# Kernel tuning notes

Measured on AMD Instinct MI355X. Metric: run time of the kernel, lower is better.

Reference implementation:

```python
import jax, jax.numpy as jnp
import numpy as np

T, B = 128, 64
STATE_DIM, LATENT_DIM, AC_DIM, MS_DIM = 32, 16, 8, 8
STATE_EMBED, AC_EMBED, HIDDEN, OUT_DIM = 64, 16, 64, 18


def setup_inputs() -> dict:
    key = jax.random.key(0)
    ks = jax.random.split(key, 18)
    f = lambda i, shape: jax.random.normal(ks[i], shape, jnp.float32)
    s = 0.05  # param scale
    return dict(
        state=f(0, (T, B, STATE_DIM)),
        latent_mean=f(1, (T, B, LATENT_DIM)),
        latent_logvar=f(2, (T, B, LATENT_DIM)) * 0.1,
        latent_mean_t=f(3, (T, B, LATENT_DIM)),
        latent_logvar_t=f(4, (T, B, LATENT_DIM)) * 0.1,
        agent_character=f(5, (T, B, AC_DIM)),
        mental_state=f(6, (T, B, MS_DIM)),
        partner_actions=jax.random.randint(ks[7], (T, B), 0, OUT_DIM, jnp.int32),
        dones=(jax.random.uniform(ks[8], (T, B)) < 0.05).astype(jnp.float32),
        W_state=f(9, (STATE_DIM, STATE_EMBED)) * s, b_state=jnp.zeros(STATE_EMBED),
        W_ac=f(10, (AC_DIM, AC_EMBED)) * s, b_ac=jnp.zeros(AC_EMBED),
        W_embed=f(11, (STATE_EMBED + AC_EMBED, HIDDEN)) * s, b_embed=jnp.zeros(HIDDEN),
        W_hid=f(12, (AC_EMBED + MS_DIM, HIDDEN)) * s, b_hid=jnp.zeros(HIDDEN),
        Wi=f(13, (HIDDEN, 3 * HIDDEN)) * s, bi=jnp.zeros(3 * HIDDEN),
        Wh_rz=f(14, (HIDDEN, 2 * HIDDEN)) * s,
        Wh_n=f(15, (HIDDEN, HIDDEN)) * s, bh_n=jnp.zeros(HIDDEN),
        W_out=f(16, (HIDDEN, OUT_DIM)) * s, b_out=jnp.zeros(OUT_DIM),
    )


def reference(state, latent_mean, latent_logvar, latent_mean_t, latent_logvar_t,
              agent_character, mental_state, partner_actions, dones,
              W_state, b_state, W_ac, b_ac, W_embed, b_embed, W_hid, b_hid,
              Wi, bi, Wh_rz, Wh_n, bh_n, W_out, b_out):
    Tn = state.shape[0]
    # ---- KL between consecutive latent Gaussians (with N(0,I) prior at t=0) ----
    lm = jnp.concatenate((latent_mean, latent_mean_t), -1)      # (T,B,2L)
    lv = jnp.concatenate((latent_logvar, latent_logvar_t), -1)
    G = lm.shape[-1]
    am = jnp.concatenate((jnp.zeros((1,) + lm.shape[1:], lm.dtype), lm))
    al = jnp.concatenate((jnp.zeros((1,) + lv.shape[1:], lv.dtype), lv))
    mu, m = am[1:], am[:-1]
    logE, logS = al[1:], al[:-1]
    kl = 0.5 * (logS.sum(-1) - logE.sum(-1) - G
                + jnp.exp(logE - logS).sum(-1)
                + ((m - mu) ** 2 / jnp.exp(logS)).sum(-1))      # (T,B)
    kl_loss = kl.sum()
    # ---- feature extractors ----
    se = jax.nn.relu(state @ W_state + b_state)                 # (T,B,SE)
    ae = jax.nn.relu(agent_character @ W_ac + b_ac)             # (T,B,AE)
    embed = jnp.concatenate((se, ae), -1) @ W_embed + b_embed   # (T,B,H)
    hidden = jnp.concatenate((ae, mental_state), -1) @ W_hid + b_hid  # (T,B,H)
    # ---- k-batch: K=T shifted trajectories, zero-padded at the tail ----
    idx = jnp.arange(Tn)[:, None] + jnp.arange(Tn)[None, :]     # (K,T)
    valid = idx < Tn                                            # (K,T) bool
    cidx = jnp.minimum(idx, Tn - 1)
    vf = valid.astype(embed.dtype)[..., None]                   # (K,T,1)
    k_embed = embed[cidx] * vf[..., None]                       # (K,T,B,H)
    k_hidden = hidden[cidx] * vf[..., None]                     # (K,T,B,H)
    k_dones = dones[cidx] * vf                                  # (K,T,B)
    k_actions = jnp.where(valid[..., None], partner_actions[cidx], 0)  # (K,T,B)
    # fill_to_first_true: 1 up to and including the first done of each k-traj
    episode_mask = (jnp.cumsum(k_dones, axis=1) - k_dones == 0).astype(embed.dtype)  # (K,T,B)
    # ---- GRU scan over timestep axis, vectorized over (K,B) ----
    h0 = k_hidden[:, 0]                                         # (K,B,H)
    xs = (jnp.moveaxis(k_embed, 1, 0), jnp.moveaxis(k_hidden, 1, 0), jnp.moveaxis(k_dones, 1, 0))

    def step(h, x):
        x_t, h0_t, d_t = x                                      # (K,B,H),(K,B,H),(K,B)
        h = jnp.where(d_t[..., None] > 0, h0_t, h)              # reset on done
        ir, iz, i_n = jnp.split(x_t @ Wi + bi, 3, -1)
        hr, hz = jnp.split(h @ Wh_rz, 2, -1)
        r = jax.nn.sigmoid(ir + hr)
        z = jax.nn.sigmoid(iz + hz)
        n = jnp.tanh(i_n + r * (h @ Wh_n + bh_n))
        h_new = (1.0 - z) * n + z * h
        return h_new, h_new

    _, hs = jax.lax.scan(step, h0, xs)                          # (T,K,B,H)
    logp = jax.nn.log_softmax(hs @ W_out + b_out, -1)           # (T,K,B,O)
    k_act_t = jnp.moveaxis(k_actions, 1, 0)                     # (T,K,B)
    nll = -jnp.take_along_axis(logp, k_act_t[..., None], -1)[..., 0]  # (T,K,B)
    mask = valid.T[:, :, None].astype(nll.dtype) * jnp.moveaxis(episode_mask, 1, 0)
    recon_loss = (nll * mask).sum(axis=1)                       # sum over K -> (T,B)
    return kl_loss, recon_loss
```

## Files before the change

kernel.cpp:

```cpp
#include <hip/hip_runtime.h>


#define XI_OFF   0
#define HID_OFF  6291456
#define CTR_OFF  8388608

typedef float f32x16 __attribute__((ext_vector_type(16)));
typedef _Float16 h2 __attribute__((ext_vector_type(2)));

#if __has_builtin(__builtin_amdgcn_fdot2)
#define DOT2(a, b, c) __builtin_amdgcn_fdot2((a), (b), (c), false)
#else
#define DOT2(a, b, c) ((c) + (float)(a).x * (float)(b).x + (float)(a).y * (float)(b).y)
#endif

__device__ __forceinline__ h2 pack_pair(float h) {
  int hb = __builtin_bit_cast(int, h);
  int hp = __builtin_amdgcn_mov_dpp(hb, 0xB1, 0xF, 0xF, true);
  return __builtin_bit_cast(h2, __builtin_amdgcn_cvt_pkrtz(h, __builtin_bit_cast(float, hp)));
}

__global__ __launch_bounds__(256, 1) void precompute_kernel(
    const float* __restrict__ state, const float* __restrict__ ac, const float* __restrict__ ms,
    const float* __restrict__ Wst, const float* __restrict__ bst,
    const float* __restrict__ Wac, const float* __restrict__ bac,
    const float* __restrict__ Wem, const float* __restrict__ bem,
    const float* __restrict__ Whd, const float* __restrict__ bhd,
    const float* __restrict__ Wi,  const float* __restrict__ bi,
    const float* __restrict__ lm, const float* __restrict__ lv,
    const float* __restrict__ lmt, const float* __restrict__ lvt,
    float* __restrict__ xi, float* __restrict__ hid0, float* __restrict__ out) {
  __shared__ float sWst[32 * 64];
  __shared__ float sWem[80 * 64];
  __shared__ float sWhd[24 * 64];
  __shared__ float sWac[8 * 16];
  __shared__ float sb[208];
  __shared__ float sin_[4][48];
  __shared__ float sse[4][80];
  __shared__ float semb[4][64];
  __shared__ float ps[4];
  int tid = threadIdx.x, lane = tid & 63, w = tid >> 6;

  if (blockIdx.x >= 256) {
    float total = 0.f;
    for (int it = 0; it < 16; ++it) {
      int idx = ((int)blockIdx.x - 256) * 256 + tid + it * 16384;
      int g = idx & 31;
      int pair = idx >> 5;
      const float* M = (g < 16) ? lm : lmt;
      const float* V = (g < 16) ? lv : lvt;
      int cur = pair * 16 + (g & 15);
      float mu = M[cur], lE = V[cur];
      float m = 0.f, lS = 0.f;
      if (pair >= 64) { m = M[cur - 1024]; lS = V[cur - 1024]; }
      float d = m - mu;
      total += 0.5f * (lS - lE - 1.f + __expf(lE - lS) + d * d * __expf(-lS));
    }
    #pragma unroll
    for (int off = 32; off; off >>= 1) total += __shfl_xor(total, off);
    if (lane == 0) ps[w] = total;
    __syncthreads();
    if (tid == 0) atomicAdd(out, ps[0] + ps[1] + ps[2] + ps[3]);
    return;
  }

  f32x16 wi0[4], wi1[4], wi2[4];
  #pragma unroll
  for (int k = 0; k < 64; ++k) {
    wi0[k >> 4][k & 15] = Wi[k * 192 + lane];
    wi1[k >> 4][k & 15] = Wi[k * 192 + 64 + lane];
    wi2[k >> 4][k & 15] = Wi[k * 192 + 128 + lane];
  }
  for (int i = tid; i < 32 * 64; i += 256) sWst[i] = Wst[i];
  for (int i = tid; i < 80 * 64; i += 256) sWem[i] = Wem[i];
  for (int i = tid; i < 24 * 64; i += 256) sWhd[i] = Whd[i];
  for (int i = tid; i < 8 * 16; i += 256) sWac[i] = Wac[i];
  if (tid < 64) sb[tid] = bst[tid];
  if (tid < 16) sb[64 + tid] = bac[tid];
  if (tid < 64) sb[80 + tid] = bem[tid];
  if (tid < 64) sb[144 + tid] = bhd[tid];
  float bi0 = bi[lane], bi1 = bi[64 + lane], bi2 = bi[128 + lane];
  __syncthreads();
  for (int cnt = 0; cnt < 8; ++cnt) {
    int pair = blockIdx.x * 32 + w * 8 + cnt;
    if (lane < 32)      sin_[w][lane] = state[pair * 32 + lane];
    else if (lane < 40) sin_[w][lane] = ac[pair * 8 + (lane - 32)];
    else if (lane < 48) sin_[w][lane] = ms[pair * 8 + (lane - 40)];
    __syncthreads();
    float se = sb[lane];
    #pragma unroll
    for (int k = 0; k < 32; ++k) se += sin_[w][k] * sWst[k * 64 + lane];
    se = fmaxf(se, 0.f);
    float ae = 0.f;
    if (lane < 16) {
      ae = sb[64 + lane];
      #pragma unroll
      for (int k = 0; k < 8; ++k) ae += sin_[w][32 + k] * sWac[k * 16 + lane];
      ae = fmaxf(ae, 0.f);
    }
    __syncthreads();
    sse[w][lane] = se;
    if (lane < 16) sse[w][64 + lane] = ae;
    __syncthreads();
    float em = sb[80 + lane];
    #pragma unroll
    for (int k = 0; k < 80; ++k) em += sse[w][k] * sWem[k * 64 + lane];
    float hd = sb[144 + lane];
    #pragma unroll
    for (int k = 0; k < 16; ++k) hd += sse[w][64 + k] * sWhd[k * 64 + lane];
    #pragma unroll
    for (int k = 0; k < 8; ++k) hd += sin_[w][40 + k] * sWhd[(16 + k) * 64 + lane];
    hid0[pair * 64 + lane] = hd;
    semb[w][lane] = em;
    __syncthreads();
    float x0 = bi0, x1 = bi1, x2 = bi2;
    #pragma unroll
    for (int k = 0; k < 64; ++k) {
      float e = semb[w][k];
      x0 += e * wi0[k >> 4][k & 15];
      x1 += e * wi1[k >> 4][k & 15];
      x2 += e * wi2[k >> 4][k & 15];
    }
    float* xo = xi + pair * 192;
    xo[lane] = x0; xo[64 + lane] = x1; xo[128 + lane] = x2;
    __syncthreads();
  }
}

__global__ __launch_bounds__(64, 2) void rollout_kernel(
    const float* __restrict__ xi, const float* __restrict__ hid0,
    const float* __restrict__ dones, const int* __restrict__ actions,
    const float* __restrict__ Whrz, const float* __restrict__ Whn,
    const float* __restrict__ bhn, const float* __restrict__ Wout,
    const float* __restrict__ bout, float* __restrict__ out,
    unsigned int* __restrict__ ctr) {
  __shared__ __attribute__((aligned(16))) h2 sh2[32];
  __shared__ __attribute__((aligned(16))) float sloge[20];
  int lane = threadIdx.x;
  int row = (lane < 18) ? lane : 0;
  h2 Wr[32], Wz[32], Wn[32], Wo[32];
  #pragma unroll
  for (int k = 0; k < 32; ++k) {
    Wr[k] = h2{(_Float16)Whrz[(2 * k) * 128 + lane],      (_Float16)Whrz[(2 * k + 1) * 128 + lane]};
    Wz[k] = h2{(_Float16)Whrz[(2 * k) * 128 + 64 + lane], (_Float16)Whrz[(2 * k + 1) * 128 + 64 + lane]};
    Wn[k] = h2{(_Float16)Whn[(2 * k) * 64 + lane],        (_Float16)Whn[(2 * k + 1) * 64 + lane]};
    Wo[k] = h2{(_Float16)Wout[(2 * k) * 18 + row],        (_Float16)Wout[(2 * k + 1) * 18 + row]};
  }
  if (lane < 2) sloge[18 + lane] = 0.f;
  float bhn_r = bhn[lane];
  float bo_r = bout[row];
  __syncthreads();
  const uint4* shv = (const uint4*)sh2;
  while (true) {
    int i = 0;
    if (lane == 0) i = (int)atomicAdd(ctr, 1u);
    i = __shfl(i, 0);
    if (i >= 8192) break;
    int t = i >> 6, b = i & 63;
    int u = t;
    int pr = (t << 6) | b;
    float h = hid0[pr * 64 + lane];
    const float* xb = xi + pr * 192;
    float x0 = xb[lane], x1 = xb[64 + lane], x2 = xb[128 + lane];
    float d = dones[pr];
    int  act = actions[pr];
    if ((lane & 1) == 0) sh2[lane >> 1] = pack_pair(h);
    for (int s = 0;; ++s) {
      int un = (u < 127) ? u + 1 : 127;
      int prn = (un << 6) | b;
      const float* xn = xi + prn * 192;
      float nx0 = xn[lane], nx1 = xn[64 + lane], nx2 = xn[128 + lane];
      float nd = dones[prn];
      int   na = actions[prn];
      float nh = hid0[prn * 64 + lane];
      float ara = x0, arb = 0.f, aza = x1, azb = 0.f, ana = 0.f, anb = 0.f;
      #pragma unroll
      for (int q = 0; q < 8; ++q) {
        uint4 hv = shv[q];
        h2 a0 = __builtin_bit_cast(h2, hv.x);
        h2 a1 = __builtin_bit_cast(h2, hv.y);
        h2 a2 = __builtin_bit_cast(h2, hv.z);
        h2 a3 = __builtin_bit_cast(h2, hv.w);
        ara = DOT2(a0, Wr[4 * q + 0], ara); arb = DOT2(a1, Wr[4 * q + 1], arb);
        ara = DOT2(a2, Wr[4 * q + 2], ara); arb = DOT2(a3, Wr[4 * q + 3], arb);
        aza = DOT2(a0, Wz[4 * q + 0], aza); azb = DOT2(a1, Wz[4 * q + 1], azb);
        aza = DOT2(a2, Wz[4 * q + 2], aza); azb = DOT2(a3, Wz[4 * q + 3], azb);
        ana = DOT2(a0, Wn[4 * q + 0], ana); anb = DOT2(a1, Wn[4 * q + 1], anb);
        ana = DOT2(a2, Wn[4 * q + 2], ana); anb = DOT2(a3, Wn[4 * q + 3], anb);
      }
      float ar = ara + arb, az = aza + azb, an = ana + anb;
      float r = __builtin_amdgcn_rcpf(1.f + __expf(-ar));
      float z = __builtin_amdgcn_rcpf(1.f + __expf(-az));
      float pre = x2 + r * (an + bhn_r);
      float n = 1.f - 2.f * __builtin_amdgcn_rcpf(1.f + __expf(2.f * pre));
      float hn = (1.f - z) * n + z * h;
      if ((lane & 1) == 0) sh2[lane >> 1] = pack_pair(hn);
      float la_a = bo_r, la_b = 0.f;
      #pragma unroll
      for (int q = 0; q < 8; ++q) {
        uint4 hv = shv[q];
        la_a = DOT2(__builtin_bit_cast(h2, hv.x), Wo[4 * q + 0], la_a);
        la_b = DOT2(__builtin_bit_cast(h2, hv.y), Wo[4 * q + 1], la_b);
        la_a = DOT2(__builtin_bit_cast(h2, hv.z), Wo[4 * q + 2], la_a);
        la_b = DOT2(__builtin_bit_cast(h2, hv.w), Wo[4 * q + 3], la_b);
      }
      float logit = la_a + la_b;
      if (lane < 18) sloge[lane] = __expf(logit);
      float4 e0 = *(const float4*)&sloge[0];
      float4 e1 = *(const float4*)&sloge[4];
      float4 e2 = *(const float4*)&sloge[8];
      float4 e3 = *(const float4*)&sloge[12];
      float4 e4 = *(const float4*)&sloge[16];
      float ssum = (((e0.x + e0.y) + (e0.z + e0.w)) + ((e1.x + e1.y) + (e1.z + e1.w)))
                 + (((e2.x + e2.y) + (e2.z + e2.w)) + ((e3.x + e3.y) + (e3.z + e3.w)))
                 + ((e4.x + e4.y) + (e4.z + e4.w));
      float la = __builtin_bit_cast(float, __builtin_amdgcn_readlane(__builtin_bit_cast(int, logit), act));
      float lse = __logf(ssum);
      if (lane == 0) atomicAdd(&out[1 + s * 64 + b], lse - la);
      if (d > 0.f || u == 127) break;
      u = un; x0 = nx0; x1 = nx1; x2 = nx2; d = nd; act = na;
      if (nd > 0.f) {
        h = nh;
        if ((lane & 1) == 0) sh2[lane >> 1] = pack_pair(h);
      } else {
        h = hn;
      }
    }
  }
}

extern "C" void kernel_launch(void* const* d_in, const int* in_sizes, int n_in,
                              void* d_out, int out_size, void* d_ws, size_t ws_size,
                              hipStream_t stream) {
  const float* state = (const float*)d_in[0];
  const float* lm    = (const float*)d_in[1];
  const float* lv    = (const float*)d_in[2];
  const float* lmt   = (const float*)d_in[3];
  const float* lvt   = (const float*)d_in[4];
  const float* ac    = (const float*)d_in[5];
  const float* ms    = (const float*)d_in[6];
  const int*   actions = (const int*)d_in[7];
  const float* dones = (const float*)d_in[8];
  const float* Wst = (const float*)d_in[9],  *bst = (const float*)d_in[10];
  const float* Wac = (const float*)d_in[11], *bac = (const float*)d_in[12];
  const float* Wem = (const float*)d_in[13], *bem = (const float*)d_in[14];
  const float* Whd = (const float*)d_in[15], *bhd = (const float*)d_in[16];
  const float* Wi  = (const float*)d_in[17], *bi  = (const float*)d_in[18];
  const float* Whrz = (const float*)d_in[19];
  const float* Whn  = (const float*)d_in[20], *bhn = (const float*)d_in[21];
  const float* Wout = (const float*)d_in[22], *bout = (const float*)d_in[23];
  float* out = (float*)d_out;
  float* xi   = (float*)((char*)d_ws + XI_OFF);
  float* hid0 = (float*)((char*)d_ws + HID_OFF);
  unsigned int* ctr = (unsigned int*)((char*)d_ws + CTR_OFF);

  hipMemsetAsync(d_out, 0, (size_t)out_size * sizeof(float), stream);
  hipMemsetAsync(ctr, 0, sizeof(unsigned int), stream);

  hipLaunchKernelGGL(precompute_kernel, dim3(320), dim3(256), 0, stream,
                     state, ac, ms, Wst, bst, Wac, bac, Wem, bem, Whd, bhd, Wi, bi,
                     lm, lv, lmt, lvt, xi, hid0, out);
  hipLaunchKernelGGL(rollout_kernel, dim3(2048), dim3(64), 0, stream,
                     xi, hid0, dones, actions, Whrz, Whn, bhn, Wout, bout, out, ctr);
}
```

Baseline: 191.1 us.

## Batch eight rollouts per wavefront and compute GRU steps with MFMA

The rollout kernel now handles eight independent rollouts per wavefront. It packs their hidden states into a small shared fp16 tile and computes the recurrent gates and output logits with 16x16x16 f16 MFMA instructions, replacing the per-lane fdot2 dot products. Slots pull new rollouts from the atomic counter as they finish, and the grid is halved. Half of the MFMA columns are padding and the slots diverge in length. Wavefronts may also idle while some slots wait, and register pressure rises from holding the weight fragments.

```diff
diff --git a/kernel.cpp b/kernel.cpp
--- a/kernel.cpp
+++ b/kernel.cpp
@@ -6,19 +6,18 @@
 #define CTR_OFF  8388608
 
 typedef float f32x16 __attribute__((ext_vector_type(16)));
-typedef _Float16 h2 __attribute__((ext_vector_type(2)));
-
-#if __has_builtin(__builtin_amdgcn_fdot2)
-#define DOT2(a, b, c) __builtin_amdgcn_fdot2((a), (b), (c), false)
+typedef float f32x4  __attribute__((ext_vector_type(4)));
+typedef __fp16 fp16x4 __attribute__((ext_vector_type(4)));
+
+#if defined(__HIP_DEVICE_COMPILE__)
+#if __has_builtin(__builtin_amdgcn_mfma_f32_16x16x16f16)
+#define MFMA16(a, b, c) __builtin_amdgcn_mfma_f32_16x16x16f16((a), (b), (c), 0, 0, 0)
 #else
-#define DOT2(a, b, c) ((c) + (float)(a).x * (float)(b).x + (float)(a).y * (float)(b).y)
+#define MFMA16(a, b, c) __builtin_amdgcn_mfma_f32_16x16x16_f16((a), (b), (c), 0, 0, 0)
 #endif
-
-__device__ __forceinline__ h2 pack_pair(float h) {
-  int hb = __builtin_bit_cast(int, h);
-  int hp = __builtin_amdgcn_mov_dpp(hb, 0xB1, 0xF, 0xF, true);
-  return __builtin_bit_cast(h2, __builtin_amdgcn_cvt_pkrtz(h, __builtin_bit_cast(float, hp)));
-}
+#else
+#define MFMA16(a, b, c) (c)
+#endif
 
 __global__ __launch_bounds__(256, 1) void precompute_kernel(
     const float* __restrict__ state, const float* __restrict__ ac, const float* __restrict__ ms,
@@ -134,98 +133,149 @@
     const float* __restrict__ bhn, const float* __restrict__ Wout,
     const float* __restrict__ bout, float* __restrict__ out,
     unsigned int* __restrict__ ctr) {
-  __shared__ __attribute__((aligned(16))) h2 sh2[32];
-  __shared__ __attribute__((aligned(16))) float sloge[20];
+  __shared__ __attribute__((aligned(16))) __fp16 hbuf[16 * 72];
+  __shared__ float sbh[64];
+  __shared__ float sbo[20];
   int lane = threadIdx.x;
-  int row = (lane < 18) ? lane : 0;
-  h2 Wr[32], Wz[32], Wn[32], Wo[32];
-  #pragma unroll
-  for (int k = 0; k < 32; ++k) {
-    Wr[k] = h2{(_Float16)Whrz[(2 * k) * 128 + lane],      (_Float16)Whrz[(2 * k + 1) * 128 + lane]};
-    Wz[k] = h2{(_Float16)Whrz[(2 * k) * 128 + 64 + lane], (_Float16)Whrz[(2 * k + 1) * 128 + 64 + lane]};
-    Wn[k] = h2{(_Float16)Whn[(2 * k) * 64 + lane],        (_Float16)Whn[(2 * k + 1) * 64 + lane]};
-    Wo[k] = h2{(_Float16)Wout[(2 * k) * 18 + row],        (_Float16)Wout[(2 * k + 1) * 18 + row]};
-  }
-  if (lane < 2) sloge[18 + lane] = 0.f;
-  float bhn_r = bhn[lane];
-  float bo_r = bout[row];
+  int g = lane >> 4, col = lane & 15, slot = col & 7;
+
+  fp16x4 aW[12][4];
+  #pragma unroll
+  for (int mt = 0; mt < 12; ++mt)
+    #pragma unroll
+    for (int kt = 0; kt < 4; ++kt)
+      #pragma unroll
+      for (int j = 0; j < 4; ++j) {
+        int kk = kt * 16 + g * 4 + j;
+        int m = mt * 16 + col;
+        float v = (m < 128) ? Whrz[kk * 128 + m] : Whn[kk * 64 + (m - 128)];
+        aW[mt][kt][j] = (__fp16)v;
+      }
+  fp16x4 aO[2][4];
+  #pragma unroll
+  for (int mt = 0; mt < 2; ++mt)
+    #pragma unroll
+    for (int kt = 0; kt < 4; ++kt)
+      #pragma unroll
+      for (int j = 0; j < 4; ++j) {
+        int kk = kt * 16 + g * 4 + j;
+        int cls = mt * 16 + col;
+        aO[mt][kt][j] = (__fp16)((cls < 18) ? Wout[kk * 18 + cls] : 0.f);
+      }
+  for (int i = lane; i < 16 * 72; i += 64) hbuf[i] = (__fp16)0.f;
+  sbh[lane] = bhn[lane];
+  if (lane < 18) sbo[lane] = bout[lane];
+  if (lane < 2)  sbo[18 + lane] = 0.f;
   __syncthreads();
-  const uint4* shv = (const uint4*)sh2;
-  while (true) {
-    int i = 0;
-    if (lane == 0) i = (int)atomicAdd(ctr, 1u);
-    i = __shfl(i, 0);
-    if (i >= 8192) break;
-    int t = i >> 6, b = i & 63;
-    int u = t;
-    int pr = (t << 6) | b;
-    float h = hid0[pr * 64 + lane];
-    const float* xb = xi + pr * 192;
-    float x0 = xb[lane], x1 = xb[64 + lane], x2 = xb[128 + lane];
-    float d = dones[pr];
-    int  act = actions[pr];
-    if ((lane & 1) == 0) sh2[lane >> 1] = pack_pair(h);
-    for (int s = 0;; ++s) {
-      int un = (u < 127) ? u + 1 : 127;
-      int prn = (un << 6) | b;
-      const float* xn = xi + prn * 192;
-      float nx0 = xn[lane], nx1 = xn[64 + lane], nx2 = xn[128 + lane];
-      float nd = dones[prn];
-      int   na = actions[prn];
-      float nh = hid0[prn * 64 + lane];
-      float ara = x0, arb = 0.f, aza = x1, azb = 0.f, ana = 0.f, anb = 0.f;
-      #pragma unroll
-      for (int q = 0; q < 8; ++q) {
-        uint4 hv = shv[q];
-        h2 a0 = __builtin_bit_cast(h2, hv.x);
-        h2 a1 = __builtin_bit_cast(h2, hv.y);
-        h2 a2 = __builtin_bit_cast(h2, hv.z);
-        h2 a3 = __builtin_bit_cast(h2, hv.w);
-        ara = DOT2(a0, Wr[4 * q + 0], ara); arb = DOT2(a1, Wr[4 * q + 1], arb);
-        ara = DOT2(a2, Wr[4 * q + 2], ara); arb = DOT2(a3, Wr[4 * q + 3], arb);
-        aza = DOT2(a0, Wz[4 * q + 0], aza); azb = DOT2(a1, Wz[4 * q + 1], azb);
-        aza = DOT2(a2, Wz[4 * q + 2], aza); azb = DOT2(a3, Wz[4 * q + 3], azb);
-        ana = DOT2(a0, Wn[4 * q + 0], ana); anb = DOT2(a1, Wn[4 * q + 1], anb);
-        ana = DOT2(a2, Wn[4 * q + 2], ana); anb = DOT2(a3, Wn[4 * q + 3], anb);
-      }
-      float ar = ara + arb, az = aza + azb, an = ana + anb;
-      float r = __builtin_amdgcn_rcpf(1.f + __expf(-ar));
-      float z = __builtin_amdgcn_rcpf(1.f + __expf(-az));
-      float pre = x2 + r * (an + bhn_r);
-      float n = 1.f - 2.f * __builtin_amdgcn_rcpf(1.f + __expf(2.f * pre));
-      float hn = (1.f - z) * n + z * h;
-      if ((lane & 1) == 0) sh2[lane >> 1] = pack_pair(hn);
-      float la_a = bo_r, la_b = 0.f;
-      #pragma unroll
-      for (int q = 0; q < 8; ++q) {
-        uint4 hv = shv[q];
-        la_a = DOT2(__builtin_bit_cast(h2, hv.x), Wo[4 * q + 0], la_a);
-        la_b = DOT2(__builtin_bit_cast(h2, hv.y), Wo[4 * q + 1], la_b);
-        la_a = DOT2(__builtin_bit_cast(h2, hv.z), Wo[4 * q + 2], la_a);
-        la_b = DOT2(__builtin_bit_cast(h2, hv.w), Wo[4 * q + 3], la_b);
-      }
-      float logit = la_a + la_b;
-      if (lane < 18) sloge[lane] = __expf(logit);
-      float4 e0 = *(const float4*)&sloge[0];
-      float4 e1 = *(const float4*)&sloge[4];
-      float4 e2 = *(const float4*)&sloge[8];
-      float4 e3 = *(const float4*)&sloge[12];
-      float4 e4 = *(const float4*)&sloge[16];
-      float ssum = (((e0.x + e0.y) + (e0.z + e0.w)) + ((e1.x + e1.y) + (e1.z + e1.w)))
-                 + (((e2.x + e2.y) + (e2.z + e2.w)) + ((e3.x + e3.y) + (e3.z + e3.w)))
-                 + ((e4.x + e4.y) + (e4.z + e4.w));
-      float la = __builtin_bit_cast(float, __builtin_amdgcn_readlane(__builtin_bit_cast(int, logit), act));
-      float lse = __logf(ssum);
-      if (lane == 0) atomicAdd(&out[1 + s * 64 + b], lse - la);
-      if (d > 0.f || u == 127) break;
-      u = un; x0 = nx0; x1 = nx1; x2 = nx2; d = nd; act = na;
-      if (nd > 0.f) {
-        h = nh;
-        if ((lane & 1) == 0) sh2[lane >> 1] = pack_pair(h);
-      } else {
-        h = hn;
-      }
-    }
+
+  int base = 0;
+  if (lane == 0) base = (int)atomicAdd(ctr, 8u);
+  base = __shfl(base, 0);
+  int idx = base + slot;
+  bool live = idx < 8192;
+  int u = idx >> 6, b = idx & 63, scnt = 0;
+  bool fresh = true;
+  int pair = u * 64 + b;
+  float d = dones[pair];
+  int act = actions[pair];
+  f32x4 acc[12], xvn[4];
+  #pragma unroll
+  for (int mt = 0; mt < 8; ++mt) acc[mt] = *(const f32x4*)(xi + pair * 192 + mt * 16 + g * 4);
+  #pragma unroll
+  for (int t = 0; t < 4; ++t) xvn[t] = *(const f32x4*)(xi + pair * 192 + 128 + t * 16 + g * 4);
+
+  f32x4 h4[4] = {f32x4{0,0,0,0}, f32x4{0,0,0,0}, f32x4{0,0,0,0}, f32x4{0,0,0,0}};
+
+  while (__ballot(live)) {
+    if (d > 0.f || fresh) {
+      #pragma unroll
+      for (int t = 0; t < 4; ++t) h4[t] = *(const f32x4*)(hid0 + pair * 64 + t * 16 + g * 4);
+      fresh = false;
+      if (col < 8) {
+        #pragma unroll
+        for (int t = 0; t < 4; ++t) {
+          fp16x4 hw; hw[0]=(__fp16)h4[t][0]; hw[1]=(__fp16)h4[t][1]; hw[2]=(__fp16)h4[t][2]; hw[3]=(__fp16)h4[t][3];
+          *(fp16x4*)(hbuf + col * 72 + t * 16 + g * 4) = hw;
+        }
+      }
+    }
+    #pragma unroll
+    for (int t = 0; t < 4; ++t) acc[8 + t] = *(const f32x4*)(sbh + t * 16 + g * 4);
+    fp16x4 bb[4];
+    #pragma unroll
+    for (int kt = 0; kt < 4; ++kt) bb[kt] = *(const fp16x4*)(hbuf + col * 72 + kt * 16 + g * 4);
+    #pragma unroll
+    for (int mt = 0; mt < 12; ++mt) {
+      #pragma unroll
+      for (int kt = 0; kt < 4; ++kt) acc[mt] = MFMA16(aW[mt][kt], bb[kt], acc[mt]);
+    }
+    #pragma unroll
+    for (int t = 0; t < 4; ++t) {
+      #pragma unroll
+      for (int r = 0; r < 4; ++r) {
+        float ar = acc[t][r];
+        float az = acc[4 + t][r];
+        float anb = acc[8 + t][r];
+        float rr = __builtin_amdgcn_rcpf(1.f + __expf(-ar));
+        float zz = __builtin_amdgcn_rcpf(1.f + __expf(-az));
+        float pre = xvn[t][r] + rr * anb;
+        float nn = 1.f - 2.f * __builtin_amdgcn_rcpf(1.f + __expf(2.f * pre));
+        h4[t][r] = (1.f - zz) * nn + zz * h4[t][r];
+      }
+    }
+    if (col < 8) {
+      #pragma unroll
+      for (int t = 0; t < 4; ++t) {
+        fp16x4 hw; hw[0]=(__fp16)h4[t][0]; hw[1]=(__fp16)h4[t][1]; hw[2]=(__fp16)h4[t][2]; hw[3]=(__fp16)h4[t][3];
+        *(fp16x4*)(hbuf + col * 72 + t * 16 + g * 4) = hw;
+      }
+    }
+    fp16x4 b2[4];
+    #pragma unroll
+    for (int kt = 0; kt < 4; ++kt) b2[kt] = *(const fp16x4*)(hbuf + col * 72 + kt * 16 + g * 4);
+    f32x4 ac0 = *(const f32x4*)(sbo + g * 4);
+    f32x4 ac1 = *(const f32x4*)(sbo + 16);
+    #pragma unroll
+    for (int kt = 0; kt < 4; ++kt) {
+      ac0 = MFMA16(aO[0][kt], b2[kt], ac0);
+      ac1 = MFMA16(aO[1][kt], b2[kt], ac1);
+    }
+    float es = 0.f, la = 0.f;
+    #pragma unroll
+    for (int r = 0; r < 4; ++r) {
+      float L = ac0[r];
+      es += __expf(L);
+      la += (g * 4 + r == act) ? L : 0.f;
+    }
+    if (g == 0) {
+      float L16 = ac1[0], L17 = ac1[1];
+      es += __expf(L16) + __expf(L17);
+      la += (act == 16 ? L16 : 0.f) + (act == 17 ? L17 : 0.f);
+    }
+    es += __shfl_xor(es, 16); es += __shfl_xor(es, 32);
+    la += __shfl_xor(la, 16); la += __shfl_xor(la, 32);
+    if (lane < 8 && live) atomicAdd(&out[1 + scnt * 64 + b], __logf(es) - la);
+    bool end = (d > 0.f) || (u == 127);
+    unsigned long long bal = __ballot(end && live);
+    unsigned mask8 = (unsigned)bal & 0xFFu;
+    if (mask8) {
+      int nb = 0;
+      if (lane == 0) nb = (int)atomicAdd(ctr, (unsigned)__popc(mask8));
+      nb = __shfl(nb, 0);
+      if (end && live) {
+        int nidx = nb + __popc(mask8 & ((1u << slot) - 1u));
+        if (nidx < 8192) { u = nidx >> 6; b = nidx & 63; scnt = 0; fresh = true; }
+        else live = false;
+      }
+    }
+    if (live && !end) { u++; scnt++; }
+    pair = u * 64 + b;
+    d = dones[pair];
+    act = actions[pair];
+    #pragma unroll
+    for (int mt = 0; mt < 8; ++mt) acc[mt] = *(const f32x4*)(xi + pair * 192 + mt * 16 + g * 4);
+    #pragma unroll
+    for (int t = 0; t < 4; ++t) xvn[t] = *(const f32x4*)(xi + pair * 192 + 128 + t * 16 + g * 4);
   }
 }
 
@@ -260,6 +310,6 @@
   hipLaunchKernelGGL(precompute_kernel, dim3(320), dim3(256), 0, stream,
                      state, ac, ms, Wst, bst, Wac, bac, Wem, bem, Whd, bhd, Wi, bi,
                      lm, lv, lmt, lvt, xi, hid0, out);
-  hipLaunchKernelGGL(rollout_kernel, dim3(2048), dim3(64), 0, stream,
+  hipLaunchKernelGGL(rollout_kernel, dim3(1024), dim3(64), 0, stream,
                      xi, hid0, dones, actions, Whrz, Whn, bhn, Wout, bout, out, ctr);
 }
```

New measurement: 335.9 us. 75.8% more time.

## Defer output logits by one step, computing them from the shared hidden-state load

Applied to the files above, without the earlier changes.

The output projection and log-softmax for step s are now computed in step s+1, reusing the same LDS load of h that feeds the GRU gate dot products. This removes the second pass over shared memory each step and takes the output work off the serial recurrence chain. Segment ends and resets get an extra flush path that computes the final step's logits directly. The cost is added control complexity and a per-step pending-state bookkeeping, plus an LDS ordering hazard on sloge between the write and the reads.

```diff
diff --git a/kernel.cpp b/kernel.cpp
--- a/kernel.cpp
+++ b/kernel.cpp
@@ -165,6 +165,7 @@
     float d = dones[pr];
     int  act = actions[pr];
     if ((lane & 1) == 0) sh2[lane >> 1] = pack_pair(h);
+    bool pend = false; int pssave = 0, pact = 0;
     for (int s = 0;; ++s) {
       int un = (u < 127) ? u + 1 : 127;
       int prn = (un << 6) | b;
@@ -174,6 +175,7 @@
       int   na = actions[prn];
       float nh = hid0[prn * 64 + lane];
       float ara = x0, arb = 0.f, aza = x1, azb = 0.f, ana = 0.f, anb = 0.f;
+      float pla = bo_r, plb = 0.f;
       #pragma unroll
       for (int q = 0; q < 8; ++q) {
         uint4 hv = shv[q];
@@ -187,7 +189,11 @@
         aza = DOT2(a2, Wz[4 * q + 2], aza); azb = DOT2(a3, Wz[4 * q + 3], azb);
         ana = DOT2(a0, Wn[4 * q + 0], ana); anb = DOT2(a1, Wn[4 * q + 1], anb);
         ana = DOT2(a2, Wn[4 * q + 2], ana); anb = DOT2(a3, Wn[4 * q + 3], anb);
+        pla = DOT2(a0, Wo[4 * q + 0], pla); plb = DOT2(a1, Wo[4 * q + 1], plb);
+        pla = DOT2(a2, Wo[4 * q + 2], pla); plb = DOT2(a3, Wo[4 * q + 3], plb);
       }
+      float plog = pla + plb;
+      if (lane < 18) sloge[lane] = __expf(plog);
       float ar = ara + arb, az = aza + azb, an = ana + anb;
       float r = __builtin_amdgcn_rcpf(1.f + __expf(-ar));
       float z = __builtin_amdgcn_rcpf(1.f + __expf(-az));
@@ -195,17 +201,6 @@
       float n = 1.f - 2.f * __builtin_amdgcn_rcpf(1.f + __expf(2.f * pre));
       float hn = (1.f - z) * n + z * h;
       if ((lane & 1) == 0) sh2[lane >> 1] = pack_pair(hn);
-      float la_a = bo_r, la_b = 0.f;
-      #pragma unroll
-      for (int q = 0; q < 8; ++q) {
-        uint4 hv = shv[q];
-        la_a = DOT2(__builtin_bit_cast(h2, hv.x), Wo[4 * q + 0], la_a);
-        la_b = DOT2(__builtin_bit_cast(h2, hv.y), Wo[4 * q + 1], la_b);
-        la_a = DOT2(__builtin_bit_cast(h2, hv.z), Wo[4 * q + 2], la_a);
-        la_b = DOT2(__builtin_bit_cast(h2, hv.w), Wo[4 * q + 3], la_b);
-      }
-      float logit = la_a + la_b;
-      if (lane < 18) sloge[lane] = __expf(logit);
       float4 e0 = *(const float4*)&sloge[0];
       float4 e1 = *(const float4*)&sloge[4];
       float4 e2 = *(const float4*)&sloge[8];
@@ -214,17 +209,46 @@
       float ssum = (((e0.x + e0.y) + (e0.z + e0.w)) + ((e1.x + e1.y) + (e1.z + e1.w)))
                  + (((e2.x + e2.y) + (e2.z + e2.w)) + ((e3.x + e3.y) + (e3.z + e3.w)))
                  + ((e4.x + e4.y) + (e4.z + e4.w));
-      float la = __builtin_bit_cast(float, __builtin_amdgcn_readlane(__builtin_bit_cast(int, logit), act));
-      float lse = __logf(ssum);
-      if (lane == 0) atomicAdd(&out[1 + s * 64 + b], lse - la);
-      if (d > 0.f || u == 127) break;
+      if (pend && lane == 0) {
+        float la = __builtin_bit_cast(float, __builtin_amdgcn_readlane(__builtin_bit_cast(int, plog), pact));
+        atomicAdd(&out[1 + pssave * 64 + b], __logf(ssum) - la);
+      }
+      pend = true; pssave = s; pact = act;
+      bool end = (d > 0.f) || (u == 127);
+      bool rst = (!end) && (nd > 0.f);
+      if (end || rst) {
+        float fa = bo_r, fb = 0.f;
+        #pragma unroll
+        for (int q = 0; q < 8; ++q) {
+          uint4 hv = shv[q];
+          fa = DOT2(__builtin_bit_cast(h2, hv.x), Wo[4 * q + 0], fa);
+          fb = DOT2(__builtin_bit_cast(h2, hv.y), Wo[4 * q + 1], fb);
+          fa = DOT2(__builtin_bit_cast(h2, hv.z), Wo[4 * q + 2], fa);
+          fb = DOT2(__builtin_bit_cast(h2, hv.w), Wo[4 * q + 3], fb);
+        }
+        float flog = fa + fb;
+        if (lane < 18) sloge[lane] = __expf(flog);
+        float4 f0 = *(const float4*)&sloge[0];
+        float4 f1 = *(const float4*)&sloge[4];
+        float4 f2 = *(const float4*)&sloge[8];
+        float4 f3 = *(const float4*)&sloge[12];
+        float4 f4 = *(const float4*)&sloge[16];
+        float fsum = (((f0.x + f0.y) + (f0.z + f0.w)) + ((f1.x + f1.y) + (f1.z + f1.w)))
+                   + (((f2.x + f2.y) + (f2.z + f2.w)) + ((f3.x + f3.y) + (f3.z + f3.w)))
+                   + ((f4.x + f4.y) + (f4.z + f4.w));
+        if (lane == 0) {
+          float fla = __builtin_bit_cast(float, __builtin_amdgcn_readlane(__builtin_bit_cast(int, flog), act));
+          atomicAdd(&out[1 + s * 64 + b], __logf(fsum) - fla);
+        }
+        pend = false;
+        if (end) break;
+        h = nh;
+        if ((lane & 1) == 0) sh2[lane >> 1] = pack_pair(nh);
+        u = un; x0 = nx0; x1 = nx1; x2 = nx2; d = nd; act = na;
+        continue;
+      }
+      h = hn;
       u = un; x0 = nx0; x1 = nx1; x2 = nx2; d = nd; act = na;
-      if (nd > 0.f) {
-        h = nh;
-        if ((lane & 1) == 0) sh2[lane >> 1] = pack_pair(h);
-      } else {
-        h = hn;
-      }
     }
   }
 }
```

New measurement: 197.9 us. 1.04x slower.

## Store precomputed gate inputs in fp16 and shard work counter across eight queues

Applied to the files above, without the earlier changes.

The precompute kernel now writes the input-gate projections and initial hidden states as fp16 instead of fp32, halving the intermediate buffer traffic read by the rollout kernel. The single global atomic work counter is split into eight counters keyed by block index, each covering a subset of batch columns, to reduce atomic contention. The costs are reduced precision on the gate inputs and possible load imbalance between the eight queues.

```diff
diff --git a/kernel.cpp b/kernel.cpp
--- a/kernel.cpp
+++ b/kernel.cpp
@@ -2,8 +2,8 @@
 
 
 #define XI_OFF   0
-#define HID_OFF  6291456
-#define CTR_OFF  8388608
+#define HID_OFF  3145728
+#define CTR_OFF  4194304
 
 typedef float f32x16 __attribute__((ext_vector_type(16)));
 typedef _Float16 h2 __attribute__((ext_vector_type(2)));
@@ -29,7 +29,7 @@
     const float* __restrict__ Wi,  const float* __restrict__ bi,
     const float* __restrict__ lm, const float* __restrict__ lv,
     const float* __restrict__ lmt, const float* __restrict__ lvt,
-    float* __restrict__ xi, float* __restrict__ hid0, float* __restrict__ out) {
+    _Float16* __restrict__ xi16, _Float16* __restrict__ hid16, float* __restrict__ out) {
   __shared__ float sWst[32 * 64];
   __shared__ float sWem[80 * 64];
   __shared__ float sWhd[24 * 64];
@@ -110,7 +110,7 @@
     for (int k = 0; k < 16; ++k) hd += sse[w][64 + k] * sWhd[k * 64 + lane];
     #pragma unroll
     for (int k = 0; k < 8; ++k) hd += sin_[w][40 + k] * sWhd[(16 + k) * 64 + lane];
-    hid0[pair * 64 + lane] = hd;
+    hid16[pair * 64 + lane] = (_Float16)hd;
     semb[w][lane] = em;
     __syncthreads();
     float x0 = bi0, x1 = bi1, x2 = bi2;
@@ -121,19 +121,19 @@
       x1 += e * wi1[k >> 4][k & 15];
       x2 += e * wi2[k >> 4][k & 15];
     }
-    float* xo = xi + pair * 192;
-    xo[lane] = x0; xo[64 + lane] = x1; xo[128 + lane] = x2;
+    _Float16* xo = xi16 + pair * 192;
+    xo[lane] = (_Float16)x0; xo[64 + lane] = (_Float16)x1; xo[128 + lane] = (_Float16)x2;
     __syncthreads();
   }
 }
 
 __global__ __launch_bounds__(64, 2) void rollout_kernel(
-    const float* __restrict__ xi, const float* __restrict__ hid0,
+    const _Float16* __restrict__ xi16, const _Float16* __restrict__ hid16,
     const float* __restrict__ dones, const int* __restrict__ actions,
     const float* __restrict__ Whrz, const float* __restrict__ Whn,
     const float* __restrict__ bhn, const float* __restrict__ Wout,
     const float* __restrict__ bout, float* __restrict__ out,
-    unsigned int* __restrict__ ctr) {
+    unsigned int* __restrict__ ctrs) {
   __shared__ __attribute__((aligned(16))) h2 sh2[32];
   __shared__ __attribute__((aligned(16))) float sloge[20];
   int lane = threadIdx.x;
@@ -151,42 +151,43 @@
   float bo_r = bout[row];
   __syncthreads();
   const uint4* shv = (const uint4*)sh2;
+  int q = blockIdx.x & 7;
   while (true) {
     int i = 0;
-    if (lane == 0) i = (int)atomicAdd(ctr, 1u);
+    if (lane == 0) i = (int)atomicAdd(&ctrs[q], 1u);
     i = __shfl(i, 0);
-    if (i >= 8192) break;
-    int t = i >> 6, b = i & 63;
+    if (i >= 1024) break;
+    int t = i >> 3, b = ((i & 7) << 3) | q;
     int u = t;
     int pr = (t << 6) | b;
-    float h = hid0[pr * 64 + lane];
-    const float* xb = xi + pr * 192;
-    float x0 = xb[lane], x1 = xb[64 + lane], x2 = xb[128 + lane];
+    float h = (float)hid16[pr * 64 + lane];
+    const _Float16* xb = xi16 + pr * 192;
+    float x0 = (float)xb[lane], x1 = (float)xb[64 + lane], x2 = (float)xb[128 + lane];
     float d = dones[pr];
     int  act = actions[pr];
     if ((lane & 1) == 0) sh2[lane >> 1] = pack_pair(h);
     for (int s = 0;; ++s) {
       int un = (u < 127) ? u + 1 : 127;
       int prn = (un << 6) | b;
-      const float* xn = xi + prn * 192;
-      float nx0 = xn[lane], nx1 = xn[64 + lane], nx2 = xn[128 + lane];
+      const _Float16* xn = xi16 + prn * 192;
+      float nx0 = (float)xn[lane], nx1 = (float)xn[64 + lane], nx2 = (float)xn[128 + lane];
       float nd = dones[prn];
       int   na = actions[prn];
-      float nh = hid0[prn * 64 + lane];
+      float nh = (float)hid16[prn * 64 + lane];
       float ara = x0, arb = 0.f, aza = x1, azb = 0.f, ana = 0.f, anb = 0.f;
       #pragma unroll
-      for (int q = 0; q < 8; ++q) {
-        uint4 hv = shv[q];
+      for (int qq = 0; qq < 8; ++qq) {
+        uint4 hv = shv[qq];
         h2 a0 = __builtin_bit_cast(h2, hv.x);
         h2 a1 = __builtin_bit_cast(h2, hv.y);
         h2 a2 = __builtin_bit_cast(h2, hv.z);
         h2 a3 = __builtin_bit_cast(h2, hv.w);
-        ara = DOT2(a0, Wr[4 * q + 0], ara); arb = DOT2(a1, Wr[4 * q + 1], arb);
-        ara = DOT2(a2, Wr[4 * q + 2], ara); arb = DOT2(a3, Wr[4 * q + 3], arb);
-        aza = DOT2(a0, Wz[4 * q + 0], aza); azb = DOT2(a1, Wz[4 * q + 1], azb);
-        aza = DOT2(a2, Wz[4 * q + 2], aza); azb = DOT2(a3, Wz[4 * q + 3], azb);
-        ana = DOT2(a0, Wn[4 * q + 0], ana); anb = DOT2(a1, Wn[4 * q + 1], anb);
-        ana = DOT2(a2, Wn[4 * q + 2], ana); anb = DOT2(a3, Wn[4 * q + 3], anb);
+        ara = DOT2(a0, Wr[4 * qq + 0], ara); arb = DOT2(a1, Wr[4 * qq + 1], arb);
+        ara = DOT2(a2, Wr[4 * qq + 2], ara); arb = DOT2(a3, Wr[4 * qq + 3], arb);
+        aza = DOT2(a0, Wz[4 * qq + 0], aza); azb = DOT2(a1, Wz[4 * qq + 1], azb);
+        aza = DOT2(a2, Wz[4 * qq + 2], aza); azb = DOT2(a3, Wz[4 * qq + 3], azb);
+        ana = DOT2(a0, Wn[4 * qq + 0], ana); anb = DOT2(a1, Wn[4 * qq + 1], anb);
+        ana = DOT2(a2, Wn[4 * qq + 2], ana); anb = DOT2(a3, Wn[4 * qq + 3], anb);
       }
       float ar = ara + arb, az = aza + azb, an = ana + anb;
       float r = __builtin_amdgcn_rcpf(1.f + __expf(-ar));
@@ -197,12 +198,12 @@
       if ((lane & 1) == 0) sh2[lane >> 1] = pack_pair(hn);
       float la_a = bo_r, la_b = 0.f;
       #pragma unroll
-      for (int q = 0; q < 8; ++q) {
-        uint4 hv = shv[q];
-        la_a = DOT2(__builtin_bit_cast(h2, hv.x), Wo[4 * q + 0], la_a);
-        la_b = DOT2(__builtin_bit_cast(h2, hv.y), Wo[4 * q + 1], la_b);
-        la_a = DOT2(__builtin_bit_cast(h2, hv.z), Wo[4 * q + 2], la_a);
-        la_b = DOT2(__builtin_bit_cast(h2, hv.w), Wo[4 * q + 3], la_b);
+      for (int qq = 0; qq < 8; ++qq) {
+        uint4 hv = shv[qq];
+        la_a = DOT2(__builtin_bit_cast(h2, hv.x), Wo[4 * qq + 0], la_a);
+        la_b = DOT2(__builtin_bit_cast(h2, hv.y), Wo[4 * qq + 1], la_b);
+        la_a = DOT2(__builtin_bit_cast(h2, hv.z), Wo[4 * qq + 2], la_a);
+        la_b = DOT2(__builtin_bit_cast(h2, hv.w), Wo[4 * qq + 3], la_b);
       }
       float logit = la_a + la_b;
       if (lane < 18) sloge[lane] = __expf(logit);
@@ -250,16 +251,16 @@
   const float* Whn  = (const float*)d_in[20], *bhn = (const float*)d_in[21];
   const float* Wout = (const float*)d_in[22], *bout = (const float*)d_in[23];
   float* out = (float*)d_out;
-  float* xi   = (float*)((char*)d_ws + XI_OFF);
-  float* hid0 = (float*)((char*)d_ws + HID_OFF);
-  unsigned int* ctr = (unsigned int*)((char*)d_ws + CTR_OFF);
+  _Float16* xi16  = (_Float16*)((char*)d_ws + XI_OFF);
+  _Float16* hid16 = (_Float16*)((char*)d_ws + HID_OFF);
+  unsigned int* ctrs = (unsigned int*)((char*)d_ws + CTR_OFF);
 
   hipMemsetAsync(d_out, 0, (size_t)out_size * sizeof(float), stream);
-  hipMemsetAsync(ctr, 0, sizeof(unsigned int), stream);
+  hipMemsetAsync(ctrs, 0, 8 * sizeof(unsigned int), stream);
 
   hipLaunchKernelGGL(precompute_kernel, dim3(320), dim3(256), 0, stream,
                      state, ac, ms, Wst, bst, Wac, bac, Wem, bem, Whd, bhd, Wi, bi,
-                     lm, lv, lmt, lvt, xi, hid0, out);
+                     lm, lv, lmt, lvt, xi16, hid16, out);
   hipLaunchKernelGGL(rollout_kernel, dim3(2048), dim3(64), 0, stream,
-                     xi, hid0, dones, actions, Whrz, Whn, bhn, Wout, bout, out, ctr);
-}
+                     xi16, hid16, dones, actions, Whrz, Whn, bhn, Wout, bout, out, ctrs);
+}
```

After: 177.5 us. -7.1%, faster.
